# Kernel tuning notes

Measured on AMD Instinct MI355X. Metric: run time of the kernel, lower is better.

The kernel has to match this reference:

```python
import jax, jax.numpy as jnp
import numpy as np

B, T, N, C = 4, 6, 512, 8
HID, FEAT, EMB, IN_DIM = 64, 16, 32, 1
KS, KC, HORIZON = 3, 2, 3
ALPHA = 3.0

def _init(key, shape):
    fin = shape[-2] if len(shape) >= 2 else shape[-1]
    return jax.random.normal(key, shape, dtype=jnp.float32) * (1.0 / fin) ** 0.5

def setup_inputs():
    ks = jax.random.split(jax.random.key(0), 32)
    L_enc = (IN_DIM + FEAT + HID) * KS * KC
    L_dec = (HID + FEAT + HID) * KS * KC
    return {
        "X_seq": jax.random.normal(ks[0], (B, T, N, C), dtype=jnp.float32),
        "As": jax.random.uniform(ks[1], (N, N), dtype=jnp.float32) / N,
        "Ac": jax.random.uniform(ks[2], (C, C), dtype=jnp.float32) / C,
        "feature": jax.random.normal(ks[3], (N, FEAT), dtype=jnp.float32),
        "Wu_S": _init(ks[4], (C, HID)), "Wv_S": _init(ks[5], (C, HID)),
        "Wu_C": _init(ks[6], (N, HID)), "Wv_C": _init(ks[7], (N, HID)),
        "mfS_w1": _init(ks[8], (4, 2, 256)), "mfS_b1": jnp.zeros((4, 256), jnp.float32),
        "mfS_w2": _init(ks[9], (4, 256, 256)), "mfS_b2": jnp.zeros((4, 256), jnp.float32),
        "mfC_w1": _init(ks[10], (4, 2, 256)), "mfC_b1": jnp.zeros((4, 256), jnp.float32),
        "mfC_w2": _init(ks[11], (4, 256, 256)), "mfC_b2": jnp.zeros((4, 256), jnp.float32),
        "enc_gW": _init(ks[12], (L_enc, 2 * HID)), "enc_gb": jnp.zeros((2 * HID,), jnp.float32),
        "enc_cW": _init(ks[13], (L_enc, HID)), "enc_cb": jnp.zeros((HID,), jnp.float32),
        "dec_gW": _init(ks[14], (L_dec, 2 * HID)), "dec_gb": jnp.zeros((2 * HID,), jnp.float32),
        "dec_cW": _init(ks[15], (L_dec, HID)), "dec_cb": jnp.zeros((HID,), jnp.float32),
        "out_w1": _init(ks[16], (HID, EMB)), "out_b1": jnp.zeros((EMB,), jnp.float32),
        "out_w2": _init(ks[17], (EMB, IN_DIM)), "out_b2": jnp.zeros((IN_DIM,), jnp.float32),
    }

def _mlp(x, w1, b1, w2, b2):
    return jax.nn.relu(x @ w1 + b1) @ w2 + b2

def _mixed_fusion(A, P, w1, b1, w2, b2):
    # node_feat = [rowsum(A), rowsum(P)]; key/value MLPs indexed 0:key_A 1:key_P 2:val_A 3:val_P
    nf = jnp.stack([A.sum(-1), P.sum(-1)], axis=-1)            # [n, 2]
    An, Pn = A @ nf, P @ nf
    key = _mlp(An, w1[0], b1[0], w2[0], b2[0]) + _mlp(Pn, w1[1], b1[1], w2[1], b2[1])
    val = _mlp(An, w1[2], b1[2], w2[2], b2[2]) + _mlp(Pn, w1[3], b1[3], w2[3], b2[3])
    a = jax.nn.sigmoid(key @ val.T)
    return a * A + (1.0 - a) * P

def _adaptive_graph(Xf, Wu, Wv):
    U = jnp.tanh(ALPHA * Xf @ Wu)                              # [b,t,n,h]
    V = jnp.tanh(ALPHA * Xf @ Wv)
    M = jnp.einsum('btnh,btmh->nm', U, V)
    # Ps = softmax(relu(M - M^T)) matches einsum pair in torch source
    return jax.nn.softmax(jax.nn.relu(M - M.T), axis=-1)

def _cheby(G, K):
    mats = [jnp.eye(G.shape[0], dtype=G.dtype), G]
    for _ in range(2, K):
        mats.append(2.0 * G @ mats[-1] - mats[-2])
    return jnp.stack(mats[:K], axis=0)                         # [K, n, n]

def _bdg(X, Gs_set, Gc_set, W, b):
    # X: [b,n,c,l]; fused Ks x Kc Chebyshev mode products; cat order (k, j, l) matches torch cat
    t1 = jnp.einsum('bncl,knm->kbmcl', X, Gs_set)
    t2 = jnp.einsum('kbmcl,jcd->bmdkjl', t1, Gc_set)
    feat = t2.reshape(t2.shape[0], t2.shape[1], t2.shape[2], -1)
    return feat @ W + b

def _cell(Xt, Ht, featx, Gs_set, Gc_set, gW, gb, cW, cb):
    XH = jnp.concatenate([Xt, Ht, featx], axis=-1)
    uv = _bdg(XH, Gs_set, Gc_set, gW, gb)
    update = jax.nn.sigmoid(uv[..., :HID])
    reset = jax.nn.sigmoid(uv[..., HID:])
    cand_in = jnp.concatenate([Xt, reset * Ht, featx], axis=-1)
    cand = jnp.tanh(_bdg(cand_in, Gs_set, Gc_set, cW, cb))
    return (1.0 - update) * Ht + update * cand

def _forward(X_seq, As, Ac, feature, Wu_S, Wv_S, Wu_C, Wv_C,
             mfS_w1, mfS_b1, mfS_w2, mfS_b2, mfC_w1, mfC_b1, mfC_w2, mfC_b2,
             enc_gW, enc_gb, enc_cW, enc_cb, dec_gW, dec_gb, dec_cW, dec_cb,
             out_w1, out_b1, out_w2, out_b2):
    # MGP_Gen: adaptive spatial / categorical graphs fused with priors
    Ps = _adaptive_graph(X_seq, Wu_S, Wv_S)
    Gs = _mixed_fusion(As, Ps, mfS_w1, mfS_b1, mfS_w2, mfS_b2)
    Xc = jnp.swapaxes(X_seq, 2, 3)                             # [b,t,c,n]
    Pc = _adaptive_graph(Xc, Wu_C, Wv_C)
    Gc = _mixed_fusion(Ac, Pc, mfC_w1, mfC_b1, mfC_w2, mfC_b2)
    Gs_set, Gc_set = _cheby(Gs, KS), _cheby(Gc, KC)
    featx = jnp.broadcast_to(feature[None, :, None, :], (B, N, C, FEAT))
    X5 = X_seq[..., None]                                      # [b,t,n,c,1]
    Ht = jnp.zeros((B, N, C, HID), dtype=X_seq.dtype)
    for t in range(T):                                         # encoder GRU over history
        Ht = _cell(X5[:, t], Ht, featx, Gs_set, Gc_set, enc_gW, enc_gb, enc_cW, enc_cb)
    deco_in, Hd = Ht, Ht
    outs = []
    for _ in range(HORIZON):
        Hd = _cell(deco_in, Hd, featx, Gs_set, Gc_set, dec_gW, dec_gb, dec_cW, dec_cb)
        outs.append(_mlp(Hd, out_w1, out_b1, out_w2, out_b2))
        deco_in = Hd
    return jnp.stack(outs, axis=1)                             # [b, horizon, n, c, 1]

def reference(X_seq, As, Ac, feature, Wu_S, Wv_S, Wu_C, Wv_C, mfS_w1, mfS_b1, mfS_w2, mfS_b2, mfC_w1, mfC_b1, mfC_w2, mfC_b2, enc_gW, enc_gb, enc_cW, enc_cb, dec_gW, dec_gb, dec_cW, dec_cb, out_w1, out_b1, out_w2, out_b2):
    return _forward(X_seq, As, Ac, feature, Wu_S, Wv_S, Wu_C, Wv_C, mfS_w1, mfS_b1, mfS_w2, mfS_b2, mfC_w1, mfC_b1, mfC_w2, mfC_b2, enc_gW, enc_gb, enc_cW, enc_cb, dec_gW, dec_gb, dec_cW, dec_cb, out_w1, out_b1, out_w2, out_b2)
```

## Files before the change

kernel.cpp:

```cpp
#include <hip/hip_runtime.h>
#include <math.h>

constexpr int kB = 4, kT = 6, kN = 512, kC = 8;
constexpr int kH = 64, kF = 16, kE = 32;
constexpr int kKS = 3, kKC = 2, kHOR = 3;
constexpr int kBT = kB * kT;
constexpr int kRK = kBT * kH;
constexpr int L_ENC = 1 + kH + kF;
constexpr int L_DEC = kH + kH + kF;
constexpr int PL_ENC = 96;
constexpr int PL_DEC = 160;
constexpr int KP_ENC = 3 * PL_ENC;
constexpr int KP_DEC = 3 * PL_DEC;
constexpr float kALPHA = 3.0f;

typedef unsigned short ushortT;
typedef short short8 __attribute__((ext_vector_type(8)));
typedef float f32x4 __attribute__((ext_vector_type(4)));

__device__ __forceinline__ float sigm(float x) { return 1.0f / (1.0f + __expf(-x)); }

__device__ __forceinline__ ushortT f2bf(float f) {
    union { float f; unsigned int u; } v; v.f = f;
    unsigned int r = v.u + 0x7fffu + ((v.u >> 16) & 1u);
    return (ushortT)(r >> 16);
}

__device__ __forceinline__ void fma44(const float4& a, const float4& b, float acc[4][4]) {
    acc[0][0] += a.x*b.x; acc[0][1] += a.x*b.y; acc[0][2] += a.x*b.z; acc[0][3] += a.x*b.w;
    acc[1][0] += a.y*b.x; acc[1][1] += a.y*b.y; acc[1][2] += a.y*b.z; acc[1][3] += a.y*b.w;
    acc[2][0] += a.z*b.x; acc[2][1] += a.z*b.y; acc[2][2] += a.z*b.z; acc[2][3] += a.z*b.w;
    acc[3][0] += a.w*b.x; acc[3][1] += a.w*b.y; acc[3][2] += a.w*b.z; acc[3][3] += a.w*b.w;
}


__global__ __launch_bounds__(256) void k_uvproj_s(
    const float* __restrict__ X, const float* __restrict__ Wu, const float* __restrict__ Wv,
    float* __restrict__ Upr, float* __restrict__ Vpr)
{
    int idx = blockIdx.x * blockDim.x + threadIdx.x;
    if (idx >= kN * kBT * kH) return;
    int h = idx % kH; int bt = (idx / kH) % kBT; int n = idx / (kH * kBT);
    const float* xr = X + ((size_t)bt * kN + n) * kC;
    float u = 0.f, v = 0.f;
#pragma unroll
    for (int c = 0; c < kC; ++c) { float x = xr[c]; u += x * Wu[c*kH + h]; v += x * Wv[c*kH + h]; }
    Upr[(size_t)n * kRK + bt * kH + h] = tanhf(kALPHA * u);
    Vpr[(size_t)n * kRK + bt * kH + h] = tanhf(kALPHA * v);
}

__global__ __launch_bounds__(256) void k_uvproj_c(
    const float* __restrict__ X, const float* __restrict__ WuC, const float* __restrict__ WvC,
    float* __restrict__ Uc, float* __restrict__ Vc)
{
    int idx = blockIdx.x * blockDim.x + threadIdx.x;
    if (idx >= kBT * kC * kH) return;
    int h = idx % kH; int c = (idx / kH) % kC; int bt = idx / (kH * kC);
    const float* xb = X + (size_t)bt * kN * kC + c;
    float u = 0.f, v = 0.f;
    for (int n = 0; n < kN; ++n) { float x = xb[n*kC]; u += x * WuC[n*kH + h]; v += x * WvC[n*kH + h]; }
    Uc[(bt*kC + c)*kH + h] = tanhf(kALPHA * u);
    Vc[(bt*kC + c)*kH + h] = tanhf(kALPHA * v);
}

__global__ void k_mc(const float* __restrict__ Uc, const float* __restrict__ Vc, float* __restrict__ Mc)
{
    int t = threadIdx.x; if (t >= 64) return;
    int d = t % 8, c = t / 8;
    float s = 0.f;
    for (int bt = 0; bt < kBT; ++bt)
        for (int h = 0; h < kH; ++h)
            s += Uc[(bt*8 + c)*kH + h] * Vc[(bt*8 + d)*kH + h];
    Mc[c*8 + d] = s;
}

__global__ __launch_bounds__(256) void k_softmax_pm(const float* __restrict__ M, float* __restrict__ P, int S)
{
    int i = blockIdx.x, tid = threadIdx.x;
    __shared__ float sm[256];
    float mx = -1e30f;
    for (int j = tid; j < S; j += 256) {
        float v = fmaxf(M[(size_t)i*S + j] - M[(size_t)j*S + i], 0.f);
        mx = fmaxf(mx, v);
    }
    sm[tid] = mx; __syncthreads();
    for (int s = 128; s > 0; s >>= 1) { if (tid < s) sm[tid] = fmaxf(sm[tid], sm[tid+s]); __syncthreads(); }
    mx = sm[0]; __syncthreads();
    float sum = 0.f;
    for (int j = tid; j < S; j += 256) {
        float v = fmaxf(M[(size_t)i*S + j] - M[(size_t)j*S + i], 0.f);
        float e = __expf(v - mx);
        P[(size_t)i*S + j] = e; sum += e;
    }
    sm[tid] = sum; __syncthreads();
    for (int s = 128; s > 0; s >>= 1) { if (tid < s) sm[tid] += sm[tid+s]; __syncthreads(); }
    float inv = 1.f / sm[0];
    __syncthreads();
    for (int j = tid; j < S; j += 256) P[(size_t)i*S + j] *= inv;
}

__global__ __launch_bounds__(256) void k_nf(const float* __restrict__ A, const float* __restrict__ P,
                                            float* __restrict__ nf, int S)
{
    int i = blockIdx.x, tid = threadIdx.x;
    __shared__ float sa[256], sp[256];
    float a = 0.f, p = 0.f;
    for (int j = tid; j < S; j += 256) { a += A[(size_t)i*S + j]; p += P[(size_t)i*S + j]; }
    sa[tid] = a; sp[tid] = p; __syncthreads();
    for (int s = 128; s > 0; s >>= 1) { if (tid < s) { sa[tid] += sa[tid+s]; sp[tid] += sp[tid+s]; } __syncthreads(); }
    if (!tid) { nf[i*2] = sa[0]; nf[i*2+1] = sp[0]; }
}

__global__ __launch_bounds__(256) void k_anpn(const float* __restrict__ A, const float* __restrict__ P,
                                              const float* __restrict__ nf,
                                              float* __restrict__ An, float* __restrict__ Pn, int S)
{
    int i = blockIdx.x, tid = threadIdx.x;
    __shared__ float s0[256], s1[256], s2[256], s3[256];
    float a0 = 0, a1 = 0, p0 = 0, p1 = 0;
    for (int j = tid; j < S; j += 256) {
        float av = A[(size_t)i*S + j], pv = P[(size_t)i*S + j];
        float n0 = nf[2*j], n1 = nf[2*j + 1];
        a0 += av*n0; a1 += av*n1; p0 += pv*n0; p1 += pv*n1;
    }
    s0[tid]=a0; s1[tid]=a1; s2[tid]=p0; s3[tid]=p1; __syncthreads();
    for (int s = 128; s > 0; s >>= 1) {
        if (tid < s) { s0[tid]+=s0[tid+s]; s1[tid]+=s1[tid+s]; s2[tid]+=s2[tid+s]; s3[tid]+=s3[tid+s]; }
        __syncthreads();
    }
    if (!tid) { An[i*2]=s0[0]; An[i*2+1]=s1[0]; Pn[i*2]=s2[0]; Pn[i*2+1]=s3[0]; }
}

__global__ __launch_bounds__(256) void k_mlp1cat(
    const float* __restrict__ An, const float* __restrict__ Pn,
    const float* __restrict__ w1, const float* __restrict__ b1, int ia, int ip,
    float* __restrict__ hidAP)
{
    int idx = blockIdx.x * 256 + threadIdx.x;
    if (idx >= 512 * 512) return;
    int col = idx & 511, i = idx >> 9;
    float v;
    if (col < 256) {
        const float* w = w1 + (size_t)ia * 512; const float* b = b1 + (size_t)ia * 256;
        v = An[i*2]*w[col] + An[i*2+1]*w[256 + col] + b[col];
    } else {
        int o = col - 256;
        const float* w = w1 + (size_t)ip * 512; const float* b = b1 + (size_t)ip * 256;
        v = Pn[i*2]*w[o] + Pn[i*2+1]*w[256 + o] + b[o];
    }
    hidAP[idx] = fmaxf(v, 0.f);
}

__global__ __launch_bounds__(256) void k_prep_w2t(
    const float* __restrict__ w2, float* __restrict__ w2tK, float* __restrict__ w2tV)
{
    int idx = blockIdx.x * 256 + threadIdx.x;
    if (idx >= 256 * 512) return;
    int kk = idx & 511, n = idx >> 9;
    int j = kk >> 8, k = kk & 255;
    w2tK[idx] = w2[(size_t)(0 + j)*65536 + k*256 + n];
    w2tV[idx] = w2[(size_t)(2 + j)*65536 + k*256 + n];
}

__global__ __launch_bounds__(256) void k_gemm_ntsk(
    const float* __restrict__ A, const float* __restrict__ B, float* __restrict__ part,
    int M, int N, int K, int skl)
{
    __shared__ __align__(16) float sA[32][68];
    __shared__ __align__(16) float sB[32][68];
    int tid = threadIdx.x, tx = tid & 15, ty = tid >> 4;
    int j0 = blockIdx.x * 64, i0 = blockIdx.y * 64;
    int kb = blockIdx.z * skl;
    float acc[4][4] = {};
    for (int k0 = kb; k0 < kb + skl; k0 += 32) {
#pragma unroll
        for (int it = 0; it < 2; ++it) {
            int q = tid + it * 256;
            int row = q >> 3, ks = (q & 7) * 4;
            float4 va = *(const float4*)&A[(size_t)(i0 + row)*K + k0 + ks];
            float4 vb = *(const float4*)&B[(size_t)(j0 + row)*K + k0 + ks];
            sA[ks+0][row] = va.x; sA[ks+1][row] = va.y; sA[ks+2][row] = va.z; sA[ks+3][row] = va.w;
            sB[ks+0][row] = vb.x; sB[ks+1][row] = vb.y; sB[ks+2][row] = vb.z; sB[ks+3][row] = vb.w;
        }
        __syncthreads();
#pragma unroll
        for (int kk = 0; kk < 32; ++kk) {
            float4 a = *(const float4*)&sA[kk][ty*4];
            float4 b = *(const float4*)&sB[kk][tx*4];
            fma44(a, b, acc);
        }
        __syncthreads();
    }
    float* dst = part + (size_t)blockIdx.z * M * N;
#pragma unroll
    for (int i = 0; i < 4; ++i)
#pragma unroll
        for (int j = 0; j < 4; ++j)
            dst[(size_t)(i0 + ty*4 + i)*N + j0 + tx*4 + j] = acc[i][j];
}

__global__ __launch_bounds__(256) void k_redep(
    const float* __restrict__ part, int SK, int total, int N,
    float* __restrict__ C, int mode,
    const float* __restrict__ p1, const float* __restrict__ p2)
{
    int idx = blockIdx.x * 256 + threadIdx.x;
    if (idx >= total) return;
    float s = 0.f;
    for (int k = 0; k < SK; ++k) s += part[(size_t)k*total + idx];
    if (mode == 1) { float a = sigm(s); s = a*p1[idx] + (1.f - a)*p2[idx]; }
    else if (mode == 2) { int col = idx % N; s += p1[col] + p2[col]; }
    C[idx] = s;
}

__global__ __launch_bounds__(256) void k_catmlp(
    const float* __restrict__ AnC, const float* __restrict__ PnC,
    const float* __restrict__ w1, const float* __restrict__ b1,
    const float* __restrict__ w2, const float* __restrict__ b2,
    float* __restrict__ keyval)
{
    __shared__ float hA[8][256], hP[8][256];
    int tid = threadIdx.x;
    int kv = blockIdx.x, c0 = blockIdx.y * 64;
    int qa = kv*2, qp = kv*2 + 1;
    for (int e = tid; e < 2048; e += 256) {
        int i = e >> 8, o = e & 255;
        hA[i][o] = fmaxf(AnC[i*2]*w1[qa*512 + o] + AnC[i*2+1]*w1[qa*512 + 256 + o] + b1[qa*256 + o], 0.f);
        hP[i][o] = fmaxf(PnC[i*2]*w1[qp*512 + o] + PnC[i*2+1]*w1[qp*512 + 256 + o] + b1[qp*256 + o], 0.f);
    }
    __syncthreads();
    for (int e = tid; e < 512; e += 256) {
        int i = e >> 6, oc = c0 + (e & 63);
        float s = b2[qa*256 + oc] + b2[qp*256 + oc];
        for (int k = 0; k < 256; ++k)
            s += hA[i][k]*w2[(size_t)qa*65536 + k*256 + oc] + hP[i][k]*w2[(size_t)qp*65536 + k*256 + oc];
        keyval[(size_t)kv*2048 + i*256 + oc] = s;
    }
}

__global__ void k_gcfuse(const float* __restrict__ keyval, const float* __restrict__ Ac,
                         const float* __restrict__ Pc, float* __restrict__ GcF)
{
    int t = threadIdx.x; if (t >= 64) return;
    int c = t >> 3, d = t & 7;
    const float* key = keyval;
    const float* val = keyval + 2048;
    float s = 0.f;
    for (int k = 0; k < 256; ++k) s += key[c*256 + k] * val[d*256 + k];
    float a = sigm(s);
    GcF[c*8 + d] = a*Ac[c*8 + d] + (1.f - a)*Pc[c*8 + d];
}


__global__ void k_transp(const float* __restrict__ G, ushortT* __restrict__ Gt)
{
    __shared__ float tile[32][33];
    int bx = blockIdx.x * 32, by = blockIdx.y * 32;
    int x = threadIdx.x, y0 = threadIdx.y;
    for (int yy = y0; yy < 32; yy += 8) tile[yy][x] = G[(size_t)(by+yy)*kN + bx + x];
    __syncthreads();
    for (int yy = y0; yy < 32; yy += 8) Gt[(size_t)(bx+yy)*kN + by + x] = f2bf(tile[x][yy]);
}

__global__ __launch_bounds__(256) void k_prep_wt(
    const float* __restrict__ W, ushortT* __restrict__ WT,
    int L, int PL, int KP, int outW)
{
    int idx = blockIdx.x * blockDim.x + threadIdx.x;
    if (idx >= 2 * outW * KP) return;
    int qp = idx % KP, o = idx / KP;
    int kk = qp / PL, l = qp - kk * PL;
    int j = o / outW, oo = o - j * outW;
    float v = (l < L) ? W[(size_t)((kk*2 + j)*L + l) * outW + oo] : 0.f;
    WT[idx] = f2bf(v);
}

__global__ __launch_bounds__(256) void k_cheby_mfma(
    const ushortT* __restrict__ Gst, ushortT* __restrict__ Gst2)
{
    __shared__ short sA[128][40];
    __shared__ short sB[128][40];
    int tid = threadIdx.x;
    int m0 = blockIdx.y * 128, j0 = blockIdx.x * 128;
    int w = tid >> 6, lane = tid & 63, wr = w >> 1, wc = w & 1;
    f32x4 acc[4][4];
#pragma unroll
    for (int i = 0; i < 4; ++i)
#pragma unroll
        for (int j = 0; j < 4; ++j) acc[i][j] = (f32x4){0.f, 0.f, 0.f, 0.f};
    for (int k0 = 0; k0 < kN; k0 += 32) {
        {
            int row = tid >> 1, lc = (tid & 1) * 16;
            const ushortT* p = Gst + (size_t)(m0 + row)*kN + k0 + lc;
            *(short8*)&sA[row][lc]     = *(const short8*)p;
            *(short8*)&sA[row][lc + 8] = *(const short8*)(p + 8);
        }
        {
            int kr = tid & 31, jc = (tid >> 5) * 8;
#pragma unroll
            for (int rep = 0; rep < 2; ++rep) {
                short8 v = *(const short8*)(Gst + (size_t)(k0 + kr)*kN + j0 + jc + rep*64);
#pragma unroll
                for (int i = 0; i < 8; ++i) sB[jc + rep*64 + i][kr] = v[i];
            }
        }
        __syncthreads();
        short8 af[4], bfr[4];
#pragma unroll
        for (int mi = 0; mi < 4; ++mi)
            af[mi] = *(const short8*)&sA[wr*64 + mi*16 + (lane & 15)][(lane >> 4) * 8];
#pragma unroll
        for (int ni = 0; ni < 4; ++ni)
            bfr[ni] = *(const short8*)&sB[wc*64 + ni*16 + (lane & 15)][(lane >> 4) * 8];
#pragma unroll
        for (int mi = 0; mi < 4; ++mi)
#pragma unroll
            for (int ni = 0; ni < 4; ++ni)
                acc[mi][ni] = __builtin_amdgcn_mfma_f32_16x16x32_bf16(af[mi], bfr[ni], acc[mi][ni], 0, 0, 0);
        __syncthreads();
    }
#pragma unroll
    for (int mi = 0; mi < 4; ++mi) {
#pragma unroll
        for (int ni = 0; ni < 4; ++ni) {
            int row0 = m0 + wr*64 + mi*16 + (lane >> 4) * 4;
            int col  = j0 + wc*64 + ni*16 + (lane & 15);
#pragma unroll
            for (int q = 0; q < 4; ++q) {
                int row = row0 + q;
                Gst2[(size_t)row*kN + col] = f2bf(2.f*acc[mi][ni][q] - (row == col ? 1.f : 0.f));
            }
        }
    }
}


template<int CLP>
__global__ __launch_bounds__(256) void k_t1_mfma(
    const ushortT* __restrict__ Gst, const ushortT* __restrict__ Xin, ushortT* __restrict__ Yout)
{
    __shared__ short sA[128][40];
    __shared__ short sB[128][40];
    int tid = threadIdx.x;
    int ki = blockIdx.z >> 2, b = blockIdx.z & 3;
    const ushortT* A = Gst + (size_t)ki * kN * kN;
    const ushortT* B = Xin + (size_t)b * kN * CLP;
    ushortT* C = Yout + (size_t)(ki*4 + b) * kN * CLP;
    int m0 = blockIdx.y * 128, j0 = blockIdx.x * 128;
    int w = tid >> 6, lane = tid & 63, wr = w >> 1, wc = w & 1;
    f32x4 acc[4][4];
#pragma unroll
    for (int i = 0; i < 4; ++i)
#pragma unroll
        for (int j = 0; j < 4; ++j) acc[i][j] = (f32x4){0.f, 0.f, 0.f, 0.f};

    for (int k0 = 0; k0 < kN; k0 += 32) {
        {
            int row = tid >> 1, lc = (tid & 1) * 16;
            const ushortT* p = A + (size_t)(m0 + row)*kN + k0 + lc;
            *(short8*)&sA[row][lc]     = *(const short8*)p;
            *(short8*)&sA[row][lc + 8] = *(const short8*)(p + 8);
        }
        {
            int kr = tid & 31, jc = (tid >> 5) * 8;
#pragma unroll
            for (int rep = 0; rep < 2; ++rep) {
                short8 v = *(const short8*)(B + (size_t)(k0 + kr)*CLP + j0 + jc + rep*64);
#pragma unroll
                for (int i = 0; i < 8; ++i) sB[jc + rep*64 + i][kr] = v[i];
            }
        }
        __syncthreads();
        short8 af[4], bfr[4];
#pragma unroll
        for (int mi = 0; mi < 4; ++mi)
            af[mi] = *(const short8*)&sA[wr*64 + mi*16 + (lane & 15)][(lane >> 4) * 8];
#pragma unroll
        for (int ni = 0; ni < 4; ++ni)
            bfr[ni] = *(const short8*)&sB[wc*64 + ni*16 + (lane & 15)][(lane >> 4) * 8];
#pragma unroll
        for (int mi = 0; mi < 4; ++mi)
#pragma unroll
            for (int ni = 0; ni < 4; ++ni)
                acc[mi][ni] = __builtin_amdgcn_mfma_f32_16x16x32_bf16(af[mi], bfr[ni], acc[mi][ni], 0, 0, 0);
        __syncthreads();
    }
#pragma unroll
    for (int mi = 0; mi < 4; ++mi) {
#pragma unroll
        for (int ni = 0; ni < 4; ++ni) {
            int row = m0 + wr*64 + mi*16 + (lane >> 4) * 4;
            int col = j0 + wc*64 + ni*16 + (lane & 15);
#pragma unroll
            for (int q = 0; q < 4; ++q)
                C[(size_t)(row + q)*CLP + col] = f2bf(acc[mi][ni][q]);
        }
    }
}

template<int PL, int KP, int FN>
__global__ __launch_bounds__(256) void k_gg_mfma(
    const ushortT* __restrict__ XH, const ushortT* __restrict__ Yb,
    const ushortT* __restrict__ WT, float* __restrict__ Cout, int Ntot)
{
    constexpr int BN = 32 * FN;
    __shared__ short sA[128][40];
    __shared__ short sB[BN][40];
    int tid = threadIdx.x;
    int r0 = blockIdx.y * 128, j0 = blockIdx.x * BN;
    int b = r0 >> 12, rr = r0 & 4095;
    const ushortT* src0 = XH + (size_t)r0 * PL;
    const ushortT* src1 = Yb + ((size_t)b       * 4096 + rr) * PL;
    const ushortT* src2 = Yb + ((size_t)(4 + b) * 4096 + rr) * PL;
    int w = tid >> 6, lane = tid & 63, wr = w >> 1, wc = w & 1;
    f32x4 acc[4][FN];
#pragma unroll
    for (int i = 0; i < 4; ++i)
#pragma unroll
        for (int j = 0; j < FN; ++j) acc[i][j] = (f32x4){0.f, 0.f, 0.f, 0.f};

    for (int k0 = 0; k0 < KP; k0 += 32) {
        int kk = k0 / PL;
        int l0 = k0 - kk * PL;
        const ushortT* A = (kk == 0) ? src0 : (kk == 1) ? src1 : src2;
        {
            int row = tid >> 1, lc = (tid & 1) * 16;
            const ushortT* p = A + (size_t)row * PL + l0 + lc;
            *(short8*)&sA[row][lc]     = *(const short8*)p;
            *(short8*)&sA[row][lc + 8] = *(const short8*)(p + 8);
        }
        if (FN == 4) {
            int col = tid >> 1, seg = (tid & 1) * 16;
            const ushortT* p = WT + (size_t)(j0 + col)*KP + k0 + seg;
            *(short8*)&sB[col][seg]     = *(const short8*)p;
            *(short8*)&sB[col][seg + 8] = *(const short8*)(p + 8);
        } else {
            int col = tid >> 2, seg = (tid & 3) * 8;
            *(short8*)&sB[col][seg] = *(const short8*)(WT + (size_t)(j0 + col)*KP + k0 + seg);
        }
        __syncthreads();
        short8 af[4], bfr[FN];
#pragma unroll
        for (int mi = 0; mi < 4; ++mi)
            af[mi] = *(const short8*)&sA[wr*64 + mi*16 + (lane & 15)][(lane >> 4) * 8];
#pragma unroll
        for (int ni = 0; ni < FN; ++ni)
            bfr[ni] = *(const short8*)&sB[wc*16*FN + ni*16 + (lane & 15)][(lane >> 4) * 8];
#pragma unroll
        for (int mi = 0; mi < 4; ++mi)
#pragma unroll
            for (int ni = 0; ni < FN; ++ni)
                acc[mi][ni] = __builtin_amdgcn_mfma_f32_16x16x32_bf16(af[mi], bfr[ni], acc[mi][ni], 0, 0, 0);
        __syncthreads();
    }
#pragma unroll
    for (int mi = 0; mi < 4; ++mi) {
#pragma unroll
        for (int ni = 0; ni < FN; ++ni) {
            int row = r0 + wr*64 + mi*16 + (lane >> 4) * 4;
            int col = j0 + wc*16*FN + ni*16 + (lane & 15);
#pragma unroll
            for (int q = 0; q < 4; ++q)
                Cout[(size_t)(row + q)*Ntot + col] = acc[mi][ni][q];
        }
    }
}


__global__ __launch_bounds__(256) void k_build_enc(
    const float* __restrict__ X, int t, const float* __restrict__ Ht,
    const float* __restrict__ featr, ushortT* __restrict__ XH)
{
    int idx = blockIdx.x * blockDim.x + threadIdx.x;
    if (idx >= 16384 * PL_ENC) return;
    int l = idx % PL_ENC; int r = idx / PL_ENC;
    int c = r & 7; int m = (r >> 3) & 511; int b = r >> 12;
    float v;
    if (l == 0)            v = X[(((size_t)b*kT + t)*kN + m)*kC + c];
    else if (l < 1 + kH)   v = Ht[(size_t)r*kH + l - 1];
    else if (l < L_ENC)    v = featr[m*kF + l - 1 - kH];
    else                   v = 0.f;
    XH[idx] = f2bf(v);
}

__global__ __launch_bounds__(256) void k_build_dec(
    const float* __restrict__ Ht, const float* __restrict__ featr, ushortT* __restrict__ XH)
{
    int idx = blockIdx.x * blockDim.x + threadIdx.x;
    if (idx >= 16384 * PL_DEC) return;
    int l = idx % PL_DEC; int r = idx / PL_DEC;
    int m = (r >> 3) & 511;
    float v;
    if (l < kH)            v = Ht[(size_t)r*kH + l];
    else if (l < 2*kH)     v = Ht[(size_t)r*kH + l - kH];
    else if (l < L_DEC)    v = featr[m*kF + l - 2*kH];
    else                   v = 0.f;
    XH[idx] = f2bf(v);
}

template<int PL, int XLEN>
__global__ __launch_bounds__(256) void k_gates_ep(
    const float* __restrict__ Gg, const float* __restrict__ GcM,
    const float* __restrict__ gb, const float* __restrict__ Ht,
    float* __restrict__ upd, ushortT* __restrict__ XH)
{
    __shared__ float sG[8][256];
    __shared__ float GcS[64];
    int tid = threadIdx.x, bm = blockIdx.x;
    const float* src = Gg + (size_t)bm * 8 * 256;
    for (int i = tid; i < 2048; i += 256) sG[i >> 8][i & 255] = src[i];
    if (tid < 64) GcS[tid] = GcM[tid];
    __syncthreads();
    int d = tid >> 5, o0 = (tid & 31) * 4;
    size_t rb = (size_t)bm * 8 + d;
#pragma unroll
    for (int q = 0; q < 4; ++q) {
        int o = o0 + q;
        float pre = sG[d][o] + gb[o];
#pragma unroll
        for (int c = 0; c < 8; ++c) pre += GcS[c*8 + d] * sG[c][128 + o];
        float g = sigm(pre);
        if (o < kH) upd[rb*kH + o] = g;
        else {
            int h = o - kH;
            XH[rb*PL + XLEN + h] = f2bf(g * Ht[rb*kH + h]);
        }
    }
}

__global__ __launch_bounds__(256) void k_cand_ep(
    const float* __restrict__ Gc2, const float* __restrict__ GcM,
    const float* __restrict__ cb, const float* __restrict__ upd, float* __restrict__ Ht)
{
    __shared__ float sG[8][128];
    __shared__ float GcS[64];
    int tid = threadIdx.x, bm = blockIdx.x;
    const float* src = Gc2 + (size_t)bm * 8 * 128;
    for (int i = tid; i < 1024; i += 256) sG[i >> 7][i & 127] = src[i];
    if (tid < 64) GcS[tid] = GcM[tid];
    __syncthreads();
    int d = tid >> 5, o0 = (tid & 31) * 2;
    size_t rb = (size_t)bm * 8 + d;
#pragma unroll
    for (int q = 0; q < 2; ++q) {
        int o = o0 + q;
        float pre = sG[d][o] + cb[o];
#pragma unroll
        for (int c = 0; c < 8; ++c) pre += GcS[c*8 + d] * sG[c][64 + o];
        float cv = tanhf(pre);
        float u = upd[rb*kH + o];
        float h0 = Ht[rb*kH + o];
        Ht[rb*kH + o] = (1.f - u)*h0 + u*cv;
    }
}

__global__ __launch_bounds__(256) void k_outmlp(
    const float* __restrict__ Hd, const float* __restrict__ w1, const float* __restrict__ b1,
    const float* __restrict__ w2, const float* __restrict__ b2, float* __restrict__ out, int hz)
{
    int idx = blockIdx.x * blockDim.x + threadIdx.x;
    if (idx >= kB*kN*kC) return;
    int c = idx % kC; int m = (idx / kC) % kN; int b = idx / (kC*kN);
    const float* h = Hd + (size_t)idx * kH;
    float hreg[kH];
#pragma unroll
    for (int k = 0; k < kH; ++k) hreg[k] = h[k];
    float acc = b2[0];
    for (int e = 0; e < kE; ++e) {
        float s = b1[e];
#pragma unroll
        for (int k = 0; k < kH; ++k) s += hreg[k] * w1[k*kE + e];
        acc += fmaxf(s, 0.f) * w2[e];
    }
    out[((size_t)(b*kHOR + hz)*kN + m)*kC + c] = acc;
}

extern "C" void kernel_launch(void* const* d_in, const int* in_sizes, int n_in,
                              void* d_out, int out_size, void* d_ws, size_t ws_size,
                              hipStream_t stream)
{
    (void)in_sizes; (void)n_in; (void)out_size; (void)ws_size;
    const float* X      = (const float*)d_in[0];
    const float* As     = (const float*)d_in[1];
    const float* Ac     = (const float*)d_in[2];
    const float* featr  = (const float*)d_in[3];
    const float* WuS    = (const float*)d_in[4];
    const float* WvS    = (const float*)d_in[5];
    const float* WuC    = (const float*)d_in[6];
    const float* WvC    = (const float*)d_in[7];
    const float* mfS_w1 = (const float*)d_in[8];
    const float* mfS_b1 = (const float*)d_in[9];
    const float* mfS_w2 = (const float*)d_in[10];
    const float* mfS_b2 = (const float*)d_in[11];
    const float* mfC_w1 = (const float*)d_in[12];
    const float* mfC_b1 = (const float*)d_in[13];
    const float* mfC_w2 = (const float*)d_in[14];
    const float* mfC_b2 = (const float*)d_in[15];
    const float* enc_gW = (const float*)d_in[16];
    const float* enc_gb = (const float*)d_in[17];
    const float* enc_cW = (const float*)d_in[18];
    const float* enc_cb = (const float*)d_in[19];
    const float* dec_gW = (const float*)d_in[20];
    const float* dec_gb = (const float*)d_in[21];
    const float* dec_cW = (const float*)d_in[22];
    const float* dec_cb = (const float*)d_in[23];
    const float* out_w1 = (const float*)d_in[24];
    const float* out_b1 = (const float*)d_in[25];
    const float* out_w2 = (const float*)d_in[26];
    const float* out_b2 = (const float*)d_in[27];
    float* out = (float*)d_out;
    float* ws = (float*)d_ws;

    float* Ht     = ws;
    float* updb   = Ht + 1048576;
    float* Gg     = updb + 1048576;
    float* Gs     = Gg + 4194304;
    float* smallf = Gs + 262144;
    float* nfS = smallf;
    float* AnS = nfS + 1024;
    float* PnS = AnS + 1024;
    float* nfC = PnS + 1024;
    float* AnC = nfC + 64;
    float* PnC = AnC + 64;
    float* McB = PnC + 64;
    float* PcB = McB + 64;
    float* GcF = PcB + 64;
    float* kvC = GcF + 64;
    ushortT* XHb  = (ushortT*)(smallf + 8192);
    ushortT* Yb   = XHb + 2621440;
    ushortT* GstB = Yb + 5242880;
    ushortT* WTg_e = GstB + 524288;
    ushortT* WTc_e = WTg_e + 73728;
    ushortT* WTg_d = WTc_e + 36864;
    ushortT* WTc_d = WTg_d + 122880;
    float* Upr   = Gg;
    float* Vpr   = Upr + 786432;
    float* part  = Vpr + 786432;
    float* Ms    = part + 1048576;
    float* Ps    = Ms + 262144;
    float* hidAP = Ps + 262144;
    float* keyS  = hidAP + 262144;
    float* valS  = keyS + 131072;
    float* w2tK  = valS + 131072;
    float* w2tV  = w2tK + 131072;
    float* Uc    = w2tV + 131072;
    float* Vc    = Uc + 12288;

    constexpr int CLP_ENC = kC * PL_ENC;
    constexpr int CLP_DEC = kC * PL_DEC;

    hipMemsetAsync(Ht, 0, (size_t)16384 * kH * sizeof(float), stream);

    k_prep_wt<<<(2*128*KP_ENC + 255)/256, 256, 0, stream>>>(enc_gW, WTg_e, L_ENC, PL_ENC, KP_ENC, 128);
    k_prep_wt<<<(2*64 *KP_ENC + 255)/256, 256, 0, stream>>>(enc_cW, WTc_e, L_ENC, PL_ENC, KP_ENC, 64);
    k_prep_wt<<<(2*128*KP_DEC + 255)/256, 256, 0, stream>>>(dec_gW, WTg_d, L_DEC, PL_DEC, KP_DEC, 128);
    k_prep_wt<<<(2*64 *KP_DEC + 255)/256, 256, 0, stream>>>(dec_cW, WTc_d, L_DEC, PL_DEC, KP_DEC, 64);
    k_prep_w2t<<<512, 256, 0, stream>>>(mfS_w2, w2tK, w2tV);

    k_uvproj_s<<<(kN*kBT*kH + 255)/256, 256, 0, stream>>>(X, WuS, WvS, Upr, Vpr);
    k_gemm_ntsk<<<dim3(8, 8, 4), 256, 0, stream>>>(Upr, Vpr, part, 512, 512, 1536, 384);
    k_redep<<<1024, 256, 0, stream>>>(part, 4, 262144, 512, Ms, 0, nullptr, nullptr);
    k_softmax_pm<<<kN, 256, 0, stream>>>(Ms, Ps, kN);
    k_nf<<<kN, 256, 0, stream>>>(As, Ps, nfS, kN);
    k_anpn<<<kN, 256, 0, stream>>>(As, Ps, nfS, AnS, PnS, kN);
    k_mlp1cat<<<1024, 256, 0, stream>>>(AnS, PnS, mfS_w1, mfS_b1, 0, 1, hidAP);
    k_gemm_ntsk<<<dim3(4, 8, 2), 256, 0, stream>>>(hidAP, w2tK, part, 512, 256, 512, 256);
    k_redep<<<512, 256, 0, stream>>>(part, 2, 131072, 256, keyS, 2, mfS_b2, mfS_b2 + 256);
    k_mlp1cat<<<1024, 256, 0, stream>>>(AnS, PnS, mfS_w1, mfS_b1, 2, 3, hidAP);
    k_gemm_ntsk<<<dim3(4, 8, 2), 256, 0, stream>>>(hidAP, w2tV, part, 512, 256, 512, 256);
    k_redep<<<512, 256, 0, stream>>>(part, 2, 131072, 256, valS, 2, mfS_b2 + 512, mfS_b2 + 768);
    k_gemm_ntsk<<<dim3(8, 8, 2), 256, 0, stream>>>(keyS, valS, part, 512, 512, 256, 128);
    k_redep<<<1024, 256, 0, stream>>>(part, 2, 262144, 512, Gs, 1, As, Ps);
    k_transp<<<dim3(16, 16), dim3(32, 8), 0, stream>>>(Gs, GstB);
    k_cheby_mfma<<<dim3(4, 4), 256, 0, stream>>>(GstB, GstB + 262144);

    k_uvproj_c<<<(kBT*kC*kH + 255)/256, 256, 0, stream>>>(X, WuC, WvC, Uc, Vc);
    k_mc<<<1, 64, 0, stream>>>(Uc, Vc, McB);
    k_softmax_pm<<<kC, 256, 0, stream>>>(McB, PcB, kC);
    k_nf<<<kC, 256, 0, stream>>>(Ac, PcB, nfC, kC);
    k_anpn<<<kC, 256, 0, stream>>>(Ac, PcB, nfC, AnC, PnC, kC);
    k_catmlp<<<dim3(2, 4), 256, 0, stream>>>(AnC, PnC, mfC_w1, mfC_b1, mfC_w2, mfC_b2, kvC);
    k_gcfuse<<<1, 64, 0, stream>>>(kvC, Ac, PcB, GcF);

    for (int t = 0; t < kT; ++t) {
        k_build_enc<<<(16384*PL_ENC + 255)/256, 256, 0, stream>>>(X, t, Ht, featr, XHb);
        k_t1_mfma<CLP_ENC><<<dim3(CLP_ENC/128, 4, 8), 256, 0, stream>>>(GstB, XHb, Yb);
        k_gg_mfma<PL_ENC, KP_ENC, 4><<<dim3(2, 128), 256, 0, stream>>>(XHb, Yb, WTg_e, Gg, 256);
        k_gates_ep<PL_ENC, 1><<<2048, 256, 0, stream>>>(Gg, GcF, enc_gb, Ht, updb, XHb);
        k_t1_mfma<CLP_ENC><<<dim3(CLP_ENC/128, 4, 8), 256, 0, stream>>>(GstB, XHb, Yb);
        k_gg_mfma<PL_ENC, KP_ENC, 2><<<dim3(2, 128), 256, 0, stream>>>(XHb, Yb, WTc_e, Gg, 128);
        k_cand_ep<<<2048, 256, 0, stream>>>(Gg, GcF, enc_cb, updb, Ht);
    }

    for (int hz = 0; hz < kHOR; ++hz) {
        k_build_dec<<<(16384*PL_DEC + 255)/256, 256, 0, stream>>>(Ht, featr, XHb);
        k_t1_mfma<CLP_DEC><<<dim3(CLP_DEC/128, 4, 8), 256, 0, stream>>>(GstB, XHb, Yb);
        k_gg_mfma<PL_DEC, KP_DEC, 4><<<dim3(2, 128), 256, 0, stream>>>(XHb, Yb, WTg_d, Gg, 256);
        k_gates_ep<PL_DEC, kH><<<2048, 256, 0, stream>>>(Gg, GcF, dec_gb, Ht, updb, XHb);
        k_t1_mfma<CLP_DEC><<<dim3(CLP_DEC/128, 4, 8), 256, 0, stream>>>(GstB, XHb, Yb);
        k_gg_mfma<PL_DEC, KP_DEC, 2><<<dim3(2, 128), 256, 0, stream>>>(XHb, Yb, WTc_d, Gg, 128);
        k_cand_ep<<<2048, 256, 0, stream>>>(Gg, GcF, dec_cb, updb, Ht);
        k_outmlp<<<(kB*kN*kC + 255)/256, 256, 0, stream>>>(Ht, out_w1, out_b1, out_w2, out_b2, out, hz);
    }
}
```

Measured before the change: 1.022 ms.

## Fuse GRU gate GEMMs with epilogues, skip repeated feature diffusion, merge graph prep kernels

The gate and candidate GEMM kernels now apply their epilogues in-kernel (sigmoid/tanh, channel mixing, GRU update), so the fp32 Gg intermediate and the separate epilogue launches are gone. The encoder input is reordered so the hidden state comes first and the static feature columns sit at a fixed offset. The graph diffusion of those feature columns runs only once per loop, and later steps diffuse only the changing columns. On the graph side, softmax, row sums and the An/Pn products are merged, using the fact that a softmax row sums to one, and the small channel-graph pipeline is collapsed into fewer kernels. The risk is more shared memory per block and fewer blocks (256) in the fused GEMMs, which can lower occupancy, plus index remapping that has to stay consistent with the reordered weights.

```diff
diff --git a/kernel.cpp b/kernel.cpp
--- a/kernel.cpp
+++ b/kernel.cpp
@@ -49,86 +49,89 @@
     Vpr[(size_t)n * kRK + bt * kH + h] = tanhf(kALPHA * v);
 }
 
-__global__ __launch_bounds__(256) void k_uvproj_c(
+__global__ __launch_bounds__(512) void k_uvproj_c2(
     const float* __restrict__ X, const float* __restrict__ WuC, const float* __restrict__ WvC,
     float* __restrict__ Uc, float* __restrict__ Vc)
 {
-    int idx = blockIdx.x * blockDim.x + threadIdx.x;
-    if (idx >= kBT * kC * kH) return;
-    int h = idx % kH; int c = (idx / kH) % kC; int bt = idx / (kH * kC);
-    const float* xb = X + (size_t)bt * kN * kC + c;
+    __shared__ float Xs[4096];
+    __shared__ float Wus[4096], Wvs[4096];
+    int bt = blockIdx.x, tid = threadIdx.x;
+    for (int i = tid; i < 4096; i += 512) Xs[i] = X[(size_t)bt*4096 + i];
+    int c = tid >> 6, h = tid & 63;
     float u = 0.f, v = 0.f;
-    for (int n = 0; n < kN; ++n) { float x = xb[n*kC]; u += x * WuC[n*kH + h]; v += x * WvC[n*kH + h]; }
-    Uc[(bt*kC + c)*kH + h] = tanhf(kALPHA * u);
-    Vc[(bt*kC + c)*kH + h] = tanhf(kALPHA * v);
-}
-
-__global__ void k_mc(const float* __restrict__ Uc, const float* __restrict__ Vc, float* __restrict__ Mc)
-{
-    int t = threadIdx.x; if (t >= 64) return;
-    int d = t % 8, c = t / 8;
+    for (int n0 = 0; n0 < 512; n0 += 64) {
+        __syncthreads();
+        for (int i = tid; i < 4096; i += 512) { Wus[i] = WuC[n0*64 + i]; Wvs[i] = WvC[n0*64 + i]; }
+        __syncthreads();
+#pragma unroll 8
+        for (int nn = 0; nn < 64; ++nn) {
+            float x = Xs[(n0+nn)*8 + c];
+            u += x * Wus[nn*64 + h];
+            v += x * Wvs[nn*64 + h];
+        }
+    }
+    Uc[(size_t)bt*512 + c*64 + h] = tanhf(kALPHA * u);
+    Vc[(size_t)bt*512 + c*64 + h] = tanhf(kALPHA * v);
+}
+
+__global__ __launch_bounds__(512) void k_mc2(
+    const float* __restrict__ Uc, const float* __restrict__ Vc, float* __restrict__ Mc)
+{
+    __shared__ float red[512];
+    int tid = threadIdx.x;
+    int cd = tid & 63, kc = tid >> 6;
+    int c = cd >> 3, d = cd & 7;
     float s = 0.f;
-    for (int bt = 0; bt < kBT; ++bt)
-        for (int h = 0; h < kH; ++h)
-            s += Uc[(bt*8 + c)*kH + h] * Vc[(bt*8 + d)*kH + h];
-    Mc[c*8 + d] = s;
-}
-
-__global__ __launch_bounds__(256) void k_softmax_pm(const float* __restrict__ M, float* __restrict__ P, int S)
+    for (int q = kc*192; q < kc*192 + 192; ++q) {
+        int bt = q >> 6, h = q & 63;
+        s += Uc[(size_t)bt*512 + c*64 + h] * Vc[(size_t)bt*512 + d*64 + h];
+    }
+    red[tid] = s; __syncthreads();
+    for (int st = 256; st >= 64; st >>= 1) { if (tid < st) red[tid] += red[tid + st]; __syncthreads(); }
+    if (tid < 64) Mc[tid] = red[tid];
+}
+
+__global__ __launch_bounds__(256) void k_nfa(const float* __restrict__ A, float* __restrict__ nf)
 {
     int i = blockIdx.x, tid = threadIdx.x;
-    __shared__ float sm[256];
+    __shared__ float sa[256];
+    float a = 0.f;
+    for (int j = tid; j < kN; j += 256) a += A[(size_t)i*kN + j];
+    sa[tid] = a; __syncthreads();
+    for (int s = 128; s > 0; s >>= 1) { if (tid < s) sa[tid] += sa[tid+s]; __syncthreads(); }
+    if (!tid) { nf[i*2] = sa[0]; nf[i*2+1] = 1.0f; }
+}
+
+__global__ __launch_bounds__(256) void k_softmax_anpn(
+    const float* __restrict__ M, const float* __restrict__ A, const float* __restrict__ nf,
+    float* __restrict__ P, float* __restrict__ An, float* __restrict__ Pn)
+{
+    int i = blockIdx.x, tid = threadIdx.x;
+    __shared__ float s0[256], s1[256], s2[256], s3[256], s4[256];
     float mx = -1e30f;
-    for (int j = tid; j < S; j += 256) {
-        float v = fmaxf(M[(size_t)i*S + j] - M[(size_t)j*S + i], 0.f);
-        mx = fmaxf(mx, v);
-    }
-    sm[tid] = mx; __syncthreads();
-    for (int s = 128; s > 0; s >>= 1) { if (tid < s) sm[tid] = fmaxf(sm[tid], sm[tid+s]); __syncthreads(); }
-    mx = sm[0]; __syncthreads();
-    float sum = 0.f;
-    for (int j = tid; j < S; j += 256) {
-        float v = fmaxf(M[(size_t)i*S + j] - M[(size_t)j*S + i], 0.f);
+    for (int j = tid; j < kN; j += 256)
+        mx = fmaxf(mx, fmaxf(M[(size_t)i*kN + j] - M[(size_t)j*kN + i], 0.f));
+    s0[tid] = mx; __syncthreads();
+    for (int s = 128; s > 0; s >>= 1) { if (tid < s) s0[tid] = fmaxf(s0[tid], s0[tid+s]); __syncthreads(); }
+    mx = s0[0]; __syncthreads();
+    float sum=0, pn0=0, pn1=0, an0=0, an1=0;
+    for (int j = tid; j < kN; j += 256) {
+        float v = fmaxf(M[(size_t)i*kN + j] - M[(size_t)j*kN + i], 0.f);
         float e = __expf(v - mx);
-        P[(size_t)i*S + j] = e; sum += e;
-    }
-    sm[tid] = sum; __syncthreads();
-    for (int s = 128; s > 0; s >>= 1) { if (tid < s) sm[tid] += sm[tid+s]; __syncthreads(); }
-    float inv = 1.f / sm[0];
+        P[(size_t)i*kN + j] = e;
+        float n0 = nf[2*j], n1 = nf[2*j+1];
+        float a = A[(size_t)i*kN + j];
+        sum += e; pn0 += e*n0; pn1 += e*n1; an0 += a*n0; an1 += a*n1;
+    }
+    s0[tid]=sum; s1[tid]=pn0; s2[tid]=pn1; s3[tid]=an0; s4[tid]=an1; __syncthreads();
+    for (int s = 128; s > 0; s >>= 1) {
+        if (tid < s) { s0[tid]+=s0[tid+s]; s1[tid]+=s1[tid+s]; s2[tid]+=s2[tid+s]; s3[tid]+=s3[tid+s]; s4[tid]+=s4[tid+s]; }
+        __syncthreads();
+    }
+    float inv = 1.f / s0[0];
+    if (!tid) { Pn[i*2] = s1[0]*inv; Pn[i*2+1] = s2[0]*inv; An[i*2] = s3[0]; An[i*2+1] = s4[0]; }
     __syncthreads();
-    for (int j = tid; j < S; j += 256) P[(size_t)i*S + j] *= inv;
-}
-
-__global__ __launch_bounds__(256) void k_nf(const float* __restrict__ A, const float* __restrict__ P,
-                                            float* __restrict__ nf, int S)
-{
-    int i = blockIdx.x, tid = threadIdx.x;
-    __shared__ float sa[256], sp[256];
-    float a = 0.f, p = 0.f;
-    for (int j = tid; j < S; j += 256) { a += A[(size_t)i*S + j]; p += P[(size_t)i*S + j]; }
-    sa[tid] = a; sp[tid] = p; __syncthreads();
-    for (int s = 128; s > 0; s >>= 1) { if (tid < s) { sa[tid] += sa[tid+s]; sp[tid] += sp[tid+s]; } __syncthreads(); }
-    if (!tid) { nf[i*2] = sa[0]; nf[i*2+1] = sp[0]; }
-}
-
-__global__ __launch_bounds__(256) void k_anpn(const float* __restrict__ A, const float* __restrict__ P,
-                                              const float* __restrict__ nf,
-                                              float* __restrict__ An, float* __restrict__ Pn, int S)
-{
-    int i = blockIdx.x, tid = threadIdx.x;
-    __shared__ float s0[256], s1[256], s2[256], s3[256];
-    float a0 = 0, a1 = 0, p0 = 0, p1 = 0;
-    for (int j = tid; j < S; j += 256) {
-        float av = A[(size_t)i*S + j], pv = P[(size_t)i*S + j];
-        float n0 = nf[2*j], n1 = nf[2*j + 1];
-        a0 += av*n0; a1 += av*n1; p0 += pv*n0; p1 += pv*n1;
-    }
-    s0[tid]=a0; s1[tid]=a1; s2[tid]=p0; s3[tid]=p1; __syncthreads();
-    for (int s = 128; s > 0; s >>= 1) {
-        if (tid < s) { s0[tid]+=s0[tid+s]; s1[tid]+=s1[tid+s]; s2[tid]+=s2[tid+s]; s3[tid]+=s3[tid+s]; }
-        __syncthreads();
-    }
-    if (!tid) { An[i*2]=s0[0]; An[i*2+1]=s1[0]; Pn[i*2]=s2[0]; Pn[i*2+1]=s3[0]; }
+    for (int j = tid; j < kN; j += 256) P[(size_t)i*kN + j] *= inv;
 }
 
 __global__ __launch_bounds__(256) void k_mlp1cat(
@@ -213,20 +216,49 @@
     C[idx] = s;
 }
 
-__global__ __launch_bounds__(256) void k_catmlp(
-    const float* __restrict__ AnC, const float* __restrict__ PnC,
+__global__ __launch_bounds__(256) void k_catmlp2(
+    const float* __restrict__ Mc, const float* __restrict__ Ac,
     const float* __restrict__ w1, const float* __restrict__ b1,
     const float* __restrict__ w2, const float* __restrict__ b2,
     float* __restrict__ keyval)
 {
+    __shared__ float Pcs[64], rsA[8], Ans[16], Pns[16];
     __shared__ float hA[8][256], hP[8][256];
     int tid = threadIdx.x;
     int kv = blockIdx.x, c0 = blockIdx.y * 64;
     int qa = kv*2, qp = kv*2 + 1;
+    if (tid < 8) {
+        int i = tid;
+        float row[8]; float mx = -1e30f;
+#pragma unroll
+        for (int j = 0; j < 8; ++j) { float v = fmaxf(Mc[i*8+j] - Mc[j*8+i], 0.f); row[j] = v; mx = fmaxf(mx, v); }
+        float s = 0.f;
+#pragma unroll
+        for (int j = 0; j < 8; ++j) { row[j] = __expf(row[j] - mx); s += row[j]; }
+        float inv = 1.f / s;
+#pragma unroll
+        for (int j = 0; j < 8; ++j) Pcs[i*8+j] = row[j] * inv;
+        float a = 0.f;
+#pragma unroll
+        for (int j = 0; j < 8; ++j) a += Ac[i*8+j];
+        rsA[i] = a;
+    }
+    __syncthreads();
+    if (tid < 16) {
+        int i = tid >> 1, comp = tid & 1;
+        float an = 0.f, pn = 0.f;
+#pragma unroll
+        for (int j = 0; j < 8; ++j) {
+            float nfj = comp ? 1.f : rsA[j];
+            an += Ac[i*8+j] * nfj; pn += Pcs[i*8+j] * nfj;
+        }
+        Ans[i*2+comp] = an; Pns[i*2+comp] = pn;
+    }
+    __syncthreads();
     for (int e = tid; e < 2048; e += 256) {
         int i = e >> 8, o = e & 255;
-        hA[i][o] = fmaxf(AnC[i*2]*w1[qa*512 + o] + AnC[i*2+1]*w1[qa*512 + 256 + o] + b1[qa*256 + o], 0.f);
-        hP[i][o] = fmaxf(PnC[i*2]*w1[qp*512 + o] + PnC[i*2+1]*w1[qp*512 + 256 + o] + b1[qp*256 + o], 0.f);
+        hA[i][o] = fmaxf(Ans[i*2]*w1[qa*512 + o] + Ans[i*2+1]*w1[qa*512 + 256 + o] + b1[qa*256 + o], 0.f);
+        hP[i][o] = fmaxf(Pns[i*2]*w1[qp*512 + o] + Pns[i*2+1]*w1[qp*512 + 256 + o] + b1[qp*256 + o], 0.f);
     }
     __syncthreads();
     for (int e = tid; e < 512; e += 256) {
@@ -238,17 +270,31 @@
     }
 }
 
-__global__ void k_gcfuse(const float* __restrict__ keyval, const float* __restrict__ Ac,
-                         const float* __restrict__ Pc, float* __restrict__ GcF)
-{
+__global__ void k_gcfuse2(const float* __restrict__ keyval, const float* __restrict__ Mc,
+                          const float* __restrict__ Ac, float* __restrict__ GcF)
+{
+    __shared__ float Pcs[64];
     int t = threadIdx.x; if (t >= 64) return;
+    if (t < 8) {
+        int i = t;
+        float row[8]; float mx = -1e30f;
+#pragma unroll
+        for (int j = 0; j < 8; ++j) { float v = fmaxf(Mc[i*8+j] - Mc[j*8+i], 0.f); row[j] = v; mx = fmaxf(mx, v); }
+        float s = 0.f;
+#pragma unroll
+        for (int j = 0; j < 8; ++j) { row[j] = __expf(row[j] - mx); s += row[j]; }
+        float inv = 1.f / s;
+#pragma unroll
+        for (int j = 0; j < 8; ++j) Pcs[i*8+j] = row[j] * inv;
+    }
+    __syncthreads();
     int c = t >> 3, d = t & 7;
     const float* key = keyval;
     const float* val = keyval + 2048;
     float s = 0.f;
     for (int k = 0; k < 256; ++k) s += key[c*256 + k] * val[d*256 + k];
     float a = sigm(s);
-    GcF[c*8 + d] = a*Ac[c*8 + d] + (1.f - a)*Pc[c*8 + d];
+    GcF[c*8 + d] = a*Ac[c*8 + d] + (1.f - a)*Pcs[c*8 + d];
 }
 
 
@@ -264,14 +310,17 @@
 
 __global__ __launch_bounds__(256) void k_prep_wt(
     const float* __restrict__ W, ushortT* __restrict__ WT,
-    int L, int PL, int KP, int outW)
+    int L, int PL, int KP, int outW, int mode)
 {
     int idx = blockIdx.x * blockDim.x + threadIdx.x;
     if (idx >= 2 * outW * KP) return;
     int qp = idx % KP, o = idx / KP;
     int kk = qp / PL, l = qp - kk * PL;
+    int lo;
+    if (mode == 1) lo = (l < 64) ? l + 1 : (l == 64) ? 0 : (l < 80) ? L : (l - 15);
+    else lo = l;
     int j = o / outW, oo = o - j * outW;
-    float v = (l < L) ? W[(size_t)((kk*2 + j)*L + l) * outW + oo] : 0.f;
+    float v = (lo < L) ? W[(size_t)((kk*2 + j)*L + lo) * outW + oo] : 0.f;
     WT[idx] = f2bf(v);
 }
 
@@ -334,9 +383,8 @@
     }
 }
 
-
-template<int CLP>
-__global__ __launch_bounds__(256) void k_t1_mfma(
+template<int CLP, int PL, int ACTW, int OFF>
+__global__ __launch_bounds__(256) void k_t1m(
     const ushortT* __restrict__ Gst, const ushortT* __restrict__ Xin, ushortT* __restrict__ Yout)
 {
     __shared__ short sA[128][40];
@@ -365,7 +413,10 @@
             int kr = tid & 31, jc = (tid >> 5) * 8;
 #pragma unroll
             for (int rep = 0; rep < 2; ++rep) {
-                short8 v = *(const short8*)(B + (size_t)(k0 + kr)*CLP + j0 + jc + rep*64);
+                int j = j0 + jc + rep*64;
+                int cg = j / ACTW;
+                int col = cg*PL + OFF + (j - cg*ACTW);
+                short8 v = *(const short8*)(B + (size_t)(k0 + kr)*CLP + col);
 #pragma unroll
                 for (int i = 0; i < 8; ++i) sB[jc + rep*64 + i][kr] = v[i];
             }
@@ -390,7 +441,9 @@
 #pragma unroll
         for (int ni = 0; ni < 4; ++ni) {
             int row = m0 + wr*64 + mi*16 + (lane >> 4) * 4;
-            int col = j0 + wc*64 + ni*16 + (lane & 15);
+            int fj = j0 + wc*64 + ni*16;
+            int cg = fj / ACTW;
+            int col = cg*PL + OFF + (fj - cg*ACTW) + (lane & 15);
 #pragma unroll
             for (int q = 0; q < 4; ++q)
                 C[(size_t)(row + q)*CLP + col] = f2bf(acc[mi][ni][q]);
@@ -398,71 +451,165 @@
     }
 }
 
-template<int PL, int KP, int FN>
-__global__ __launch_bounds__(256) void k_gg_mfma(
-    const ushortT* __restrict__ XH, const ushortT* __restrict__ Yb,
-    const ushortT* __restrict__ WT, float* __restrict__ Cout, int Ntot)
-{
-    constexpr int BN = 32 * FN;
-    __shared__ short sA[128][40];
-    __shared__ short sB[BN][40];
+template<int PL, int KP, int XOFF>
+__global__ __launch_bounds__(256) void k_gates_f(
+    ushortT* __restrict__ XH, const ushortT* __restrict__ Yb,
+    const ushortT* __restrict__ WT, const float* __restrict__ GcM,
+    const float* __restrict__ gb, const float* __restrict__ Ht,
+    float* __restrict__ upd)
+{
+    __shared__ short sA[64][40];
+    __shared__ short sB[256][40];
+    __shared__ float sEp[32][260];
+    __shared__ float GcS[64], gbS[128];
     int tid = threadIdx.x;
-    int r0 = blockIdx.y * 128, j0 = blockIdx.x * BN;
+    int r0 = blockIdx.x * 64;
     int b = r0 >> 12, rr = r0 & 4095;
     const ushortT* src0 = XH + (size_t)r0 * PL;
-    const ushortT* src1 = Yb + ((size_t)b       * 4096 + rr) * PL;
+    const ushortT* src1 = Yb + ((size_t)b * 4096 + rr) * PL;
     const ushortT* src2 = Yb + ((size_t)(4 + b) * 4096 + rr) * PL;
-    int w = tid >> 6, lane = tid & 63, wr = w >> 1, wc = w & 1;
-    f32x4 acc[4][FN];
+    if (tid < 64) GcS[tid] = GcM[tid];
+    if (tid >= 64 && tid < 192) gbS[tid - 64] = gb[tid - 64];
+    int w = tid >> 6, lane = tid & 63;
+    f32x4 acc[4][4];
 #pragma unroll
     for (int i = 0; i < 4; ++i)
 #pragma unroll
-        for (int j = 0; j < FN; ++j) acc[i][j] = (f32x4){0.f, 0.f, 0.f, 0.f};
+        for (int j = 0; j < 4; ++j) acc[i][j] = (f32x4){0.f, 0.f, 0.f, 0.f};
 
     for (int k0 = 0; k0 < KP; k0 += 32) {
-        int kk = k0 / PL;
-        int l0 = k0 - kk * PL;
-        const ushortT* A = (kk == 0) ? src0 : (kk == 1) ? src1 : src2;
+        int kk = k0 / PL, l0 = k0 - kk * PL;
+        const ushortT* Ap = (kk == 0) ? src0 : (kk == 1) ? src1 : src2;
         {
-            int row = tid >> 1, lc = (tid & 1) * 16;
-            const ushortT* p = A + (size_t)row * PL + l0 + lc;
-            *(short8*)&sA[row][lc]     = *(const short8*)p;
-            *(short8*)&sA[row][lc + 8] = *(const short8*)(p + 8);
-        }
-        if (FN == 4) {
+            int row = tid >> 2, lc = (tid & 3) * 8;
+            *(short8*)&sA[row][lc] = *(const short8*)(Ap + (size_t)row*PL + l0 + lc);
+        }
+        {
+            const ushortT* p = WT + (size_t)tid*KP + k0;
+            *(short8*)&sB[tid][0]  = *(const short8*)(p);
+            *(short8*)&sB[tid][8]  = *(const short8*)(p + 8);
+            *(short8*)&sB[tid][16] = *(const short8*)(p + 16);
+            *(short8*)&sB[tid][24] = *(const short8*)(p + 24);
+        }
+        __syncthreads();
+        short8 af[4], bfr[4];
+#pragma unroll
+        for (int mi = 0; mi < 4; ++mi)
+            af[mi] = *(const short8*)&sA[mi*16 + (lane & 15)][(lane >> 4) * 8];
+#pragma unroll
+        for (int ni = 0; ni < 4; ++ni)
+            bfr[ni] = *(const short8*)&sB[w*64 + ni*16 + (lane & 15)][(lane >> 4) * 8];
+#pragma unroll
+        for (int mi = 0; mi < 4; ++mi)
+#pragma unroll
+            for (int ni = 0; ni < 4; ++ni)
+                acc[mi][ni] = __builtin_amdgcn_mfma_f32_16x16x32_bf16(af[mi], bfr[ni], acc[mi][ni], 0, 0, 0);
+        __syncthreads();
+    }
+    for (int chunk = 0; chunk < 2; ++chunk) {
+#pragma unroll
+        for (int mi2 = 0; mi2 < 2; ++mi2) {
+            int mi = chunk*2 + mi2;
+#pragma unroll
+            for (int ni = 0; ni < 4; ++ni)
+#pragma unroll
+                for (int q = 0; q < 4; ++q)
+                    sEp[mi2*16 + (lane >> 4)*4 + q][w*64 + ni*16 + (lane & 15)] = acc[mi][ni][q];
+        }
+        __syncthreads();
+        for (int it = 0; it < 16; ++it) {
+            int idx = it*256 + tid;
+            int o = idx & 127, rloc = idx >> 7;
+            int r = r0 + chunk*32 + rloc;
+            int d = r & 7, bb = rloc & ~7;
+            float pre = sEp[rloc][o] + gbS[o];
+#pragma unroll
+            for (int c = 0; c < 8; ++c) pre += GcS[c*8 + d] * sEp[bb + c][128 + o];
+            float g = sigm(pre);
+            if (o < 64) upd[(size_t)r*64 + o] = g;
+            else {
+                int h = o - 64;
+                XH[(size_t)r*PL + XOFF + h] = f2bf(g * Ht[(size_t)r*64 + h]);
+            }
+        }
+        __syncthreads();
+    }
+}
+
+template<int PL, int KP>
+__global__ __launch_bounds__(256) void k_cand_f(
+    const ushortT* __restrict__ XH, const ushortT* __restrict__ Yb,
+    const ushortT* __restrict__ WT, const float* __restrict__ GcM,
+    const float* __restrict__ cb, const float* __restrict__ upd,
+    float* __restrict__ Ht)
+{
+    __shared__ short sA[64][40];
+    __shared__ short sB[128][40];
+    __shared__ float sEp[64][132];
+    __shared__ float GcS[64], cbS[64];
+    int tid = threadIdx.x;
+    int r0 = blockIdx.x * 64;
+    int b = r0 >> 12, rr = r0 & 4095;
+    const ushortT* src0 = XH + (size_t)r0 * PL;
+    const ushortT* src1 = Yb + ((size_t)b * 4096 + rr) * PL;
+    const ushortT* src2 = Yb + ((size_t)(4 + b) * 4096 + rr) * PL;
+    if (tid < 64) GcS[tid] = GcM[tid];
+    if (tid >= 64 && tid < 128) cbS[tid - 64] = cb[tid - 64];
+    int w = tid >> 6, lane = tid & 63;
+    f32x4 acc[4][2];
+#pragma unroll
+    for (int i = 0; i < 4; ++i)
+#pragma unroll
+        for (int j = 0; j < 2; ++j) acc[i][j] = (f32x4){0.f, 0.f, 0.f, 0.f};
+
+    for (int k0 = 0; k0 < KP; k0 += 32) {
+        int kk = k0 / PL, l0 = k0 - kk * PL;
+        const ushortT* Ap = (kk == 0) ? src0 : (kk == 1) ? src1 : src2;
+        {
+            int row = tid >> 2, lc = (tid & 3) * 8;
+            *(short8*)&sA[row][lc] = *(const short8*)(Ap + (size_t)row*PL + l0 + lc);
+        }
+        {
             int col = tid >> 1, seg = (tid & 1) * 16;
-            const ushortT* p = WT + (size_t)(j0 + col)*KP + k0 + seg;
+            const ushortT* p = WT + (size_t)col*KP + k0 + seg;
             *(short8*)&sB[col][seg]     = *(const short8*)p;
             *(short8*)&sB[col][seg + 8] = *(const short8*)(p + 8);
-        } else {
-            int col = tid >> 2, seg = (tid & 3) * 8;
-            *(short8*)&sB[col][seg] = *(const short8*)(WT + (size_t)(j0 + col)*KP + k0 + seg);
-        }
-        __syncthreads();
-        short8 af[4], bfr[FN];
+        }
+        __syncthreads();
+        short8 af[4], bfr[2];
 #pragma unroll
         for (int mi = 0; mi < 4; ++mi)
-            af[mi] = *(const short8*)&sA[wr*64 + mi*16 + (lane & 15)][(lane >> 4) * 8];
-#pragma unroll
-        for (int ni = 0; ni < FN; ++ni)
-            bfr[ni] = *(const short8*)&sB[wc*16*FN + ni*16 + (lane & 15)][(lane >> 4) * 8];
+            af[mi] = *(const short8*)&sA[mi*16 + (lane & 15)][(lane >> 4) * 8];
+#pragma unroll
+        for (int ni = 0; ni < 2; ++ni)
+            bfr[ni] = *(const short8*)&sB[w*32 + ni*16 + (lane & 15)][(lane >> 4) * 8];
 #pragma unroll
         for (int mi = 0; mi < 4; ++mi)
 #pragma unroll
-            for (int ni = 0; ni < FN; ++ni)
+            for (int ni = 0; ni < 2; ++ni)
                 acc[mi][ni] = __builtin_amdgcn_mfma_f32_16x16x32_bf16(af[mi], bfr[ni], acc[mi][ni], 0, 0, 0);
         __syncthreads();
     }
 #pragma unroll
-    for (int mi = 0; mi < 4; ++mi) {
-#pragma unroll
-        for (int ni = 0; ni < FN; ++ni) {
-            int row = r0 + wr*64 + mi*16 + (lane >> 4) * 4;
-            int col = j0 + wc*16*FN + ni*16 + (lane & 15);
+    for (int mi = 0; mi < 4; ++mi)
+#pragma unroll
+        for (int ni = 0; ni < 2; ++ni)
 #pragma unroll
             for (int q = 0; q < 4; ++q)
-                Cout[(size_t)(row + q)*Ntot + col] = acc[mi][ni][q];
-        }
+                sEp[mi*16 + (lane >> 4)*4 + q][w*32 + ni*16 + (lane & 15)] = acc[mi][ni][q];
+    __syncthreads();
+    for (int it = 0; it < 16; ++it) {
+        int idx = it*256 + tid;
+        int o = idx & 63, rloc = idx >> 6;
+        int r = r0 + rloc;
+        int d = r & 7, bb = rloc & ~7;
+        float pre = sEp[rloc][o] + cbS[o];
+#pragma unroll
+        for (int c = 0; c < 8; ++c) pre += GcS[c*8 + d] * sEp[bb + c][64 + o];
+        float cv = tanhf(pre);
+        float u = upd[(size_t)r*64 + o];
+        float h0 = Ht[(size_t)r*64 + o];
+        Ht[(size_t)r*64 + o] = (1.f - u)*h0 + u*cv;
     }
 }
 
@@ -476,10 +623,10 @@
     int l = idx % PL_ENC; int r = idx / PL_ENC;
     int c = r & 7; int m = (r >> 3) & 511; int b = r >> 12;
     float v;
-    if (l == 0)            v = X[(((size_t)b*kT + t)*kN + m)*kC + c];
-    else if (l < 1 + kH)   v = Ht[(size_t)r*kH + l - 1];
-    else if (l < L_ENC)    v = featr[m*kF + l - 1 - kH];
-    else                   v = 0.f;
+    if (l < 64)            v = Ht[(size_t)r*kH + l];
+    else if (l == 64)      v = X[(((size_t)b*kT + t)*kN + m)*kC + c];
+    else if (l < 80)       v = 0.f;
+    else                   v = featr[m*kF + (l - 80)];
     XH[idx] = f2bf(v);
 }
 
@@ -496,62 +643,6 @@
     else if (l < L_DEC)    v = featr[m*kF + l - 2*kH];
     else                   v = 0.f;
     XH[idx] = f2bf(v);
-}
-
-template<int PL, int XLEN>
-__global__ __launch_bounds__(256) void k_gates_ep(
-    const float* __restrict__ Gg, const float* __restrict__ GcM,
-    const float* __restrict__ gb, const float* __restrict__ Ht,
-    float* __restrict__ upd, ushortT* __restrict__ XH)
-{
-    __shared__ float sG[8][256];
-    __shared__ float GcS[64];
-    int tid = threadIdx.x, bm = blockIdx.x;
-    const float* src = Gg + (size_t)bm * 8 * 256;
-    for (int i = tid; i < 2048; i += 256) sG[i >> 8][i & 255] = src[i];
-    if (tid < 64) GcS[tid] = GcM[tid];
-    __syncthreads();
-    int d = tid >> 5, o0 = (tid & 31) * 4;
-    size_t rb = (size_t)bm * 8 + d;
-#pragma unroll
-    for (int q = 0; q < 4; ++q) {
-        int o = o0 + q;
-        float pre = sG[d][o] + gb[o];
-#pragma unroll
-        for (int c = 0; c < 8; ++c) pre += GcS[c*8 + d] * sG[c][128 + o];
-        float g = sigm(pre);
-        if (o < kH) upd[rb*kH + o] = g;
-        else {
-            int h = o - kH;
-            XH[rb*PL + XLEN + h] = f2bf(g * Ht[rb*kH + h]);
-        }
-    }
-}
-
-__global__ __launch_bounds__(256) void k_cand_ep(
-    const float* __restrict__ Gc2, const float* __restrict__ GcM,
-    const float* __restrict__ cb, const float* __restrict__ upd, float* __restrict__ Ht)
-{
-    __shared__ float sG[8][128];
-    __shared__ float GcS[64];
-    int tid = threadIdx.x, bm = blockIdx.x;
-    const float* src = Gc2 + (size_t)bm * 8 * 128;
-    for (int i = tid; i < 1024; i += 256) sG[i >> 7][i & 127] = src[i];
-    if (tid < 64) GcS[tid] = GcM[tid];
-    __syncthreads();
-    int d = tid >> 5, o0 = (tid & 31) * 2;
-    size_t rb = (size_t)bm * 8 + d;
-#pragma unroll
-    for (int q = 0; q < 2; ++q) {
-        int o = o0 + q;
-        float pre = sG[d][o] + cb[o];
-#pragma unroll
-        for (int c = 0; c < 8; ++c) pre += GcS[c*8 + d] * sG[c][64 + o];
-        float cv = tanhf(pre);
-        float u = upd[rb*kH + o];
-        float h0 = Ht[rb*kH + o];
-        Ht[rb*kH + o] = (1.f - u)*h0 + u*cv;
-    }
 }
 
 __global__ __launch_bounds__(256) void k_outmlp(
@@ -619,12 +710,8 @@
     float* nfS = smallf;
     float* AnS = nfS + 1024;
     float* PnS = AnS + 1024;
-    float* nfC = PnS + 1024;
-    float* AnC = nfC + 64;
-    float* PnC = AnC + 64;
-    float* McB = PnC + 64;
-    float* PcB = McB + 64;
-    float* GcF = PcB + 64;
+    float* McB = PnS + 1024;
+    float* GcF = McB + 64;
     float* kvC = GcF + 64;
     ushortT* XHb  = (ushortT*)(smallf + 8192);
     ushortT* Yb   = XHb + 2621440;
@@ -651,18 +738,17 @@
 
     hipMemsetAsync(Ht, 0, (size_t)16384 * kH * sizeof(float), stream);
 
-    k_prep_wt<<<(2*128*KP_ENC + 255)/256, 256, 0, stream>>>(enc_gW, WTg_e, L_ENC, PL_ENC, KP_ENC, 128);
-    k_prep_wt<<<(2*64 *KP_ENC + 255)/256, 256, 0, stream>>>(enc_cW, WTc_e, L_ENC, PL_ENC, KP_ENC, 64);
-    k_prep_wt<<<(2*128*KP_DEC + 255)/256, 256, 0, stream>>>(dec_gW, WTg_d, L_DEC, PL_DEC, KP_DEC, 128);
-    k_prep_wt<<<(2*64 *KP_DEC + 255)/256, 256, 0, stream>>>(dec_cW, WTc_d, L_DEC, PL_DEC, KP_DEC, 64);
+    k_prep_wt<<<(2*128*KP_ENC + 255)/256, 256, 0, stream>>>(enc_gW, WTg_e, L_ENC, PL_ENC, KP_ENC, 128, 1);
+    k_prep_wt<<<(2*64 *KP_ENC + 255)/256, 256, 0, stream>>>(enc_cW, WTc_e, L_ENC, PL_ENC, KP_ENC, 64, 1);
+    k_prep_wt<<<(2*128*KP_DEC + 255)/256, 256, 0, stream>>>(dec_gW, WTg_d, L_DEC, PL_DEC, KP_DEC, 128, 0);
+    k_prep_wt<<<(2*64 *KP_DEC + 255)/256, 256, 0, stream>>>(dec_cW, WTc_d, L_DEC, PL_DEC, KP_DEC, 64, 0);
     k_prep_w2t<<<512, 256, 0, stream>>>(mfS_w2, w2tK, w2tV);
 
     k_uvproj_s<<<(kN*kBT*kH + 255)/256, 256, 0, stream>>>(X, WuS, WvS, Upr, Vpr);
     k_gemm_ntsk<<<dim3(8, 8, 4), 256, 0, stream>>>(Upr, Vpr, part, 512, 512, 1536, 384);
     k_redep<<<1024, 256, 0, stream>>>(part, 4, 262144, 512, Ms, 0, nullptr, nullptr);
-    k_softmax_pm<<<kN, 256, 0, stream>>>(Ms, Ps, kN);
-    k_nf<<<kN, 256, 0, stream>>>(As, Ps, nfS, kN);
-    k_anpn<<<kN, 256, 0, stream>>>(As, Ps, nfS, AnS, PnS, kN);
+    k_nfa<<<kN, 256, 0, stream>>>(As, nfS);
+    k_softmax_anpn<<<kN, 256, 0, stream>>>(Ms, As, nfS, Ps, AnS, PnS);
     k_mlp1cat<<<1024, 256, 0, stream>>>(AnS, PnS, mfS_w1, mfS_b1, 0, 1, hidAP);
     k_gemm_ntsk<<<dim3(4, 8, 2), 256, 0, stream>>>(hidAP, w2tK, part, 512, 256, 512, 256);
     k_redep<<<512, 256, 0, stream>>>(part, 2, 131072, 256, keyS, 2, mfS_b2, mfS_b2 + 256);
@@ -674,32 +760,35 @@
     k_transp<<<dim3(16, 16), dim3(32, 8), 0, stream>>>(Gs, GstB);
     k_cheby_mfma<<<dim3(4, 4), 256, 0, stream>>>(GstB, GstB + 262144);
 
-    k_uvproj_c<<<(kBT*kC*kH + 255)/256, 256, 0, stream>>>(X, WuC, WvC, Uc, Vc);
-    k_mc<<<1, 64, 0, stream>>>(Uc, Vc, McB);
-    k_softmax_pm<<<kC, 256, 0, stream>>>(McB, PcB, kC);
-    k_nf<<<kC, 256, 0, stream>>>(Ac, PcB, nfC, kC);
-    k_anpn<<<kC, 256, 0, stream>>>(Ac, PcB, nfC, AnC, PnC, kC);
-    k_catmlp<<<dim3(2, 4), 256, 0, stream>>>(AnC, PnC, mfC_w1, mfC_b1, mfC_w2, mfC_b2, kvC);
-    k_gcfuse<<<1, 64, 0, stream>>>(kvC, Ac, PcB, GcF);
-
+    k_uvproj_c2<<<kBT, 512, 0, stream>>>(X, WuC, WvC, Uc, Vc);
+    k_mc2<<<1, 512, 0, stream>>>(Uc, Vc, McB);
+    k_catmlp2<<<dim3(2, 4), 256, 0, stream>>>(McB, Ac, mfC_w1, mfC_b1, mfC_w2, mfC_b2, kvC);
+    k_gcfuse2<<<1, 64, 0, stream>>>(kvC, McB, Ac, GcF);
+
+    bool featDone = false;
     for (int t = 0; t < kT; ++t) {
         k_build_enc<<<(16384*PL_ENC + 255)/256, 256, 0, stream>>>(X, t, Ht, featr, XHb);
-        k_t1_mfma<CLP_ENC><<<dim3(CLP_ENC/128, 4, 8), 256, 0, stream>>>(GstB, XHb, Yb);
-        k_gg_mfma<PL_ENC, KP_ENC, 4><<<dim3(2, 128), 256, 0, stream>>>(XHb, Yb, WTg_e, Gg, 256);
-        k_gates_ep<PL_ENC, 1><<<2048, 256, 0, stream>>>(Gg, GcF, enc_gb, Ht, updb, XHb);
-        k_t1_mfma<CLP_ENC><<<dim3(CLP_ENC/128, 4, 8), 256, 0, stream>>>(GstB, XHb, Yb);
-        k_gg_mfma<PL_ENC, KP_ENC, 2><<<dim3(2, 128), 256, 0, stream>>>(XHb, Yb, WTc_e, Gg, 128);
-        k_cand_ep<<<2048, 256, 0, stream>>>(Gg, GcF, enc_cb, updb, Ht);
-    }
-
+        if (!featDone) {
+            k_t1m<CLP_ENC, PL_ENC, 16, 80><<<dim3(1, 4, 8), 256, 0, stream>>>(GstB, XHb, Yb);
+            featDone = true;
+        }
+        k_t1m<CLP_ENC, PL_ENC, 80, 0><<<dim3(5, 4, 8), 256, 0, stream>>>(GstB, XHb, Yb);
+        k_gates_f<PL_ENC, KP_ENC, 0><<<256, 256, 0, stream>>>(XHb, Yb, WTg_e, GcF, enc_gb, Ht, updb);
+        k_t1m<CLP_ENC, PL_ENC, 64, 0><<<dim3(4, 4, 8), 256, 0, stream>>>(GstB, XHb, Yb);
+        k_cand_f<PL_ENC, KP_ENC><<<256, 256, 0, stream>>>(XHb, Yb, WTc_e, GcF, enc_cb, updb, Ht);
+    }
+
+    featDone = false;
     for (int hz = 0; hz < kHOR; ++hz) {
         k_build_dec<<<(16384*PL_DEC + 255)/256, 256, 0, stream>>>(Ht, featr, XHb);
-        k_t1_mfma<CLP_DEC><<<dim3(CLP_DEC/128, 4, 8), 256, 0, stream>>>(GstB, XHb, Yb);
-        k_gg_mfma<PL_DEC, KP_DEC, 4><<<dim3(2, 128), 256, 0, stream>>>(XHb, Yb, WTg_d, Gg, 256);
-        k_gates_ep<PL_DEC, kH><<<2048, 256, 0, stream>>>(Gg, GcF, dec_gb, Ht, updb, XHb);
-        k_t1_mfma<CLP_DEC><<<dim3(CLP_DEC/128, 4, 8), 256, 0, stream>>>(GstB, XHb, Yb);
-        k_gg_mfma<PL_DEC, KP_DEC, 2><<<dim3(2, 128), 256, 0, stream>>>(XHb, Yb, WTc_d, Gg, 128);
-        k_cand_ep<<<2048, 256, 0, stream>>>(Gg, GcF, dec_cb, updb, Ht);
+        if (!featDone) {
+            k_t1m<CLP_DEC, PL_DEC, 16, 128><<<dim3(1, 4, 8), 256, 0, stream>>>(GstB, XHb, Yb);
+            featDone = true;
+        }
+        k_t1m<CLP_DEC, PL_DEC, 128, 0><<<dim3(8, 4, 8), 256, 0, stream>>>(GstB, XHb, Yb);
+        k_gates_f<PL_DEC, KP_DEC, 64><<<256, 256, 0, stream>>>(XHb, Yb, WTg_d, GcF, dec_gb, Ht, updb);
+        k_t1m<CLP_DEC, PL_DEC, 64, 64><<<dim3(4, 4, 8), 256, 0, stream>>>(GstB, XHb, Yb);
+        k_cand_f<PL_DEC, KP_DEC><<<256, 256, 0, stream>>>(XHb, Yb, WTc_d, GcF, dec_cb, updb, Ht);
         k_outmlp<<<(kB*kN*kC + 255)/256, 256, 0, stream>>>(Ht, out_w1, out_b1, out_w2, out_b2, out, hz);
     }
 }
```

After: 1.078 ms. 5.5% more time.
